# Kernel tuning notes

Hardware: AMD Instinct MI355X
Metric: run time of the kernel (lower is better)

## Reference

```python
import jax, jax.numpy as jnp
import numpy as np

T, B, N = 512, 256, 128


def setup_inputs() -> dict:
    key = jax.random.key(0)
    k1, k2, k3, k4, k5, k6 = jax.random.split(key, 6)
    emit = jax.random.normal(k1, (T, B, N), dtype=jnp.float32)
    target = jax.random.randint(k2, (T, B), 0, N, dtype=jnp.int32)
    # monotone mask: each sequence has length in [T//2, T]
    lengths = jax.random.randint(k3, (B,), T // 2, T + 1, dtype=jnp.int32)
    mask = jnp.arange(T, dtype=jnp.int32)[:, None] < lengths[None, :]
    trans = 0.1 * jax.random.normal(k4, (N, N), dtype=jnp.float32)
    strans = 0.1 * jax.random.normal(k5, (N,), dtype=jnp.float32)
    etrans = 0.1 * jax.random.normal(k6, (N,), dtype=jnp.float32)
    return {"emit": emit, "target": target, "mask": mask,
            "trans": trans, "strans": strans, "etrans": etrans}


def _crf_nll(emit, trans, strans, etrans, target, mask):
    t_len, b, n = emit.shape

    # ---- logZ: forward algorithm (sequential scan over time) ----
    def step(alpha, inp):
        emit_i, mask_i = inp  # [B,N], [B]
        # scores[b, j, k] = alpha[b, j] + trans[j, k] + emit_i[b, k]
        scores = jax.nn.logsumexp(
            alpha[:, :, None] + trans[None, :, :] + emit_i[:, None, :], axis=1)
        alpha = jnp.where(mask_i[:, None], scores, alpha)
        return alpha, None

    alpha0 = strans[None, :] + emit[0]  # [B,N]
    alpha, _ = jax.lax.scan(step, alpha0, (emit[1:], mask[1:]))
    logZ = jax.nn.logsumexp(alpha + etrans[None, :], axis=1).sum()

    # ---- gold score ----
    emit_sc = jnp.take_along_axis(emit, target[:, :, None], axis=2)[..., 0]  # [T,B]
    trans_sc = trans[target[:-1], target[1:]]  # [T-1,B]
    scores = emit_sc.at[1:].add(trans_sc)
    score = jnp.where(mask, scores, 0.0).sum()
    ends = mask.sum(axis=0) - 1  # [B]
    score = score + strans[target[0]].sum()
    score = score + etrans[target[ends, jnp.arange(b)]].sum()

    return (logZ - score) / b


def reference(emit, target, mask, trans, strans, etrans):
    return _crf_nll(emit, trans, strans, etrans, target, mask)
```

## Files before the change

### kernel.cpp

```cpp
#include <hip/hip_runtime.h>

#define T_LEN 512
#define B_SZ  256
#define N_ST  128

#if defined(__has_builtin)
# if __has_builtin(__builtin_amdgcn_fdot2_f32_bf16)
#  define HAVE_DOT2 1
# endif
#endif
#ifndef HAVE_DOT2
# define HAVE_DOT2 0
#endif

typedef unsigned int uint32;
typedef __bf16 bf16x2 __attribute__((ext_vector_type(2)));

__device__ __forceinline__ uint32 bf16rn(float f) {
    uint32 u = __builtin_bit_cast(uint32, f);
    u += 0x7fffu + ((u >> 16) & 1u);
    return u >> 16;
}
__device__ __forceinline__ uint32 pack2(float lo, float hi) {
    return bf16rn(lo) | (bf16rn(hi) << 16);
}
__device__ __forceinline__ uint32 cvtpk(float lo, float hi) {
    uint32 r;
    asm("v_cvt_pk_bf16_f32 %0, %1, %2" : "=v"(r) : "v"(lo), "v"(hi));
    return r;
}
__device__ __forceinline__ float readlane0(float v) {
    return __builtin_bit_cast(float, (uint32)__builtin_amdgcn_readlane(__builtin_bit_cast(int, v), 0));
}
__device__ __forceinline__ float dot2b(uint32 a, uint32 b, float c) {
#if HAVE_DOT2
    return __builtin_amdgcn_fdot2_f32_bf16(__builtin_bit_cast(bf16x2, a),
                                           __builtin_bit_cast(bf16x2, b), c, false);
#else
    float alo = __builtin_bit_cast(float, a << 16);
    float ahi = __builtin_bit_cast(float, a & 0xffff0000u);
    float blo = __builtin_bit_cast(float, b << 16);
    float bhi = __builtin_bit_cast(float, b & 0xffff0000u);
    return fmaf(ahi, bhi, fmaf(alo, blo, c));
#endif
}


__global__ __launch_bounds__(64) void lengths_kernel(const unsigned char* __restrict__ mask_raw,
                                                     int* __restrict__ lens) {
    int b = blockIdx.x;
    int l = threadIdx.x;
    unsigned char b1 = mask_raw[1], b2 = mask_raw[2];
    int mode = (b1 != 0) ? 0 : ((b2 != 0) ? 2 : 1);
    int cnt = 0;
    if (mode == 0) {
        #pragma unroll
        for (int k = 0; k < 8; ++k) cnt += (mask_raw[(l * 8 + k) * B_SZ + b] != 0);
    } else if (mode == 1) {
        const int* m = (const int*)mask_raw;
        #pragma unroll
        for (int k = 0; k < 8; ++k) cnt += (m[(l * 8 + k) * B_SZ + b] != 0);
    } else {
        const float* m = (const float*)mask_raw;
        #pragma unroll
        for (int k = 0; k < 8; ++k) cnt += (m[(l * 8 + k) * B_SZ + b] != 0.0f);
    }
    #pragma unroll
    for (int off = 1; off < 64; off <<= 1) cnt += __shfl_xor(cnt, off);
    if (l == 0) lens[b] = cnt;
}

__global__ void __attribute__((amdgpu_flat_work_group_size(128, 128), amdgpu_waves_per_eu(1, 1)))
forward_kernel(
        const float* __restrict__ emit,
        const float* __restrict__ trans,
        const float* __restrict__ strans,
        const float* __restrict__ etrans,
        const int* __restrict__ lens,
        float* __restrict__ logZ_out) {
    const int b   = blockIdx.x;
    const int tid = threadIdx.x;
    const int wid = tid >> 6;
    const int l   = tid & 63;
    const int c0  = 2 * l, c1 = 2 * l + 1;

    __shared__ alignas(16) uint32 a32[64];
    __shared__ alignas(16) uint32 z32[64];
    __shared__ float meetA[N_ST], meetY[N_ST];
    __shared__ float maccSh[2], red2[2];

    const int len = lens[b];
    const int m = (len - 1 < 256) ? (len - 1) : 256;
    const float* eb = emit + (size_t)b * N_ST;
    const size_t TS = (size_t)B_SZ * N_ST;

    if (wid == 0) {
        uint32 EA[64], EB[64];
        #pragma unroll
        for (int p = 0; p < 64; ++p) {
            EA[p] = pack2(__expf(trans[(2 * p) * N_ST + c0]), __expf(trans[(2 * p + 1) * N_ST + c0]));
            EB[p] = pack2(__expf(trans[(2 * p) * N_ST + c1]), __expf(trans[(2 * p + 1) * N_ST + c1]));
        }
        float aA = __expf(strans[c0] + eb[c0]);
        float aB = __expf(strans[c1] + eb[c1]);
        a32[l] = pack2(aA, aB);
        float Macc = 0.f, inv = 1.0f;
        float ec0 = eb[TS + c0],      ec1 = eb[TS + c1];
        float en0 = eb[2 * TS + c0],  en1 = eb[2 * TS + c1];
        for (int t = 1; t <= m; ++t) {
            const size_t t2 = (size_t)((t + 2 <= m) ? t + 2 : m) * TS;
            const float e20 = eb[t2 + c0], e21 = eb[t2 + c1];
            const float ee0 = __expf(ec0), ee1 = __expf(ec1);
            float A0 = 0, A1 = 0, A2 = 0, A3 = 0, B0 = 0, B1 = 0, B2 = 0, B3 = 0;
            #pragma unroll
            for (int q = 0; q < 16; ++q) {
                uint4 w;
                __builtin_memcpy(&w, (const char*)a32 + 16 * q, 16);
                A0 = dot2b(w.x, EA[4 * q + 0], A0);  B0 = dot2b(w.x, EB[4 * q + 0], B0);
                A1 = dot2b(w.y, EA[4 * q + 1], A1);  B1 = dot2b(w.y, EB[4 * q + 1], B1);
                A2 = dot2b(w.z, EA[4 * q + 2], A2);  B2 = dot2b(w.z, EB[4 * q + 2], B2);
                A3 = dot2b(w.w, EA[4 * q + 3], A3);  B3 = dot2b(w.w, EB[4 * q + 3], B3);
            }
            const float rA = (A0 + A1) + (A2 + A3);
            const float rB = (B0 + B1) + (B2 + B3);
            Macc -= __logf(inv);
            aA = ee0 * rA * inv;
            aB = ee1 * rB * inv;
            a32[l] = cvtpk(aA, aB);
            inv = __builtin_amdgcn_rcpf(readlane0(rA));
            ec0 = en0; ec1 = en1; en0 = e20; en1 = e21;
        }
        meetA[c0] = aA; meetA[c1] = aB;
        if (l == 0) maccSh[0] = Macc;
    } else {
        uint32 RA[64], RB[64];
        #pragma unroll
        for (int p = 0; p < 64; ++p) {
            RA[p] = pack2(__expf(trans[c0 * N_ST + 2 * p]), __expf(trans[c0 * N_ST + 2 * p + 1]));
            RB[p] = pack2(__expf(trans[c1 * N_ST + 2 * p]), __expf(trans[c1 * N_ST + 2 * p + 1]));
        }
        float y0 = __expf(etrans[c0]);
        float y1 = __expf(etrans[c1]);
        float Maccb = 0.f, invb = 1.0f;
        const int t0 = len - 1;
        float ec0 = eb[(size_t)t0 * TS + c0], ec1 = eb[(size_t)t0 * TS + c1];
        float en0 = ec0, en1 = ec1;
        if (t0 - 1 > m) { en0 = eb[(size_t)(t0 - 1) * TS + c0]; en1 = eb[(size_t)(t0 - 1) * TS + c1]; }
        for (int t = t0; t > m; --t) {
            const int tp = (t - 2 > m) ? t - 2 : m + 1;
            const float e20 = eb[(size_t)tp * TS + c0], e21 = eb[(size_t)tp * TS + c1];
            const float ee0 = __expf(ec0), ee1 = __expf(ec1);
            z32[l] = cvtpk(ee0 * y0, ee1 * y1);
            float R0 = 0, R1 = 0, R2 = 0, R3 = 0, S0 = 0, S1 = 0, S2 = 0, S3 = 0;
            #pragma unroll
            for (int q = 0; q < 16; ++q) {
                uint4 w;
                __builtin_memcpy(&w, (const char*)z32 + 16 * q, 16);
                R0 = dot2b(w.x, RA[4 * q + 0], R0);  S0 = dot2b(w.x, RB[4 * q + 0], S0);
                R1 = dot2b(w.y, RA[4 * q + 1], R1);  S1 = dot2b(w.y, RB[4 * q + 1], S1);
                R2 = dot2b(w.z, RA[4 * q + 2], R2);  S2 = dot2b(w.z, RB[4 * q + 2], S2);
                R3 = dot2b(w.w, RA[4 * q + 3], R3);  S3 = dot2b(w.w, RB[4 * q + 3], S3);
            }
            const float rR = (R0 + R1) + (R2 + R3);
            const float rS = (S0 + S1) + (S2 + S3);
            Maccb -= __logf(invb);
            y0 = rR * invb;
            y1 = rS * invb;
            invb = __builtin_amdgcn_rcpf(readlane0(rR));
            ec0 = en0; ec1 = en1; en0 = e20; en1 = e21;
        }
        meetY[c0] = y0; meetY[c1] = y1;
        if (l == 0) maccSh[1] = Maccb;
    }

    __syncthreads();
    float v = meetA[tid] * meetY[tid];
    #pragma unroll
    for (int off = 1; off < 64; off <<= 1) v += __shfl_xor(v, off);
    if (l == 0) red2[wid] = v;
    __syncthreads();
    if (tid == 0) logZ_out[b] = maccSh[0] + maccSh[1] + __logf(red2[0] + red2[1]);
}

__global__ __launch_bounds__(128) void score_kernel(
        const float* __restrict__ emit,
        const int* __restrict__ target,
        const float* __restrict__ trans,
        const float* __restrict__ strans,
        const float* __restrict__ etrans,
        const int* __restrict__ lens,
        float* __restrict__ score_out) {
    const int b   = blockIdx.x;
    const int tid = threadIdx.x;
    const int len = lens[b];
    float local = 0.f;
    for (int t = tid; t < len; t += 128) {
        int tgt = target[t * B_SZ + b];
        float v = emit[(size_t)t * (B_SZ * N_ST) + b * N_ST + tgt];
        if (t > 0) v += trans[target[(t - 1) * B_SZ + b] * N_ST + tgt];
        local += v;
    }
    if (tid == 0) {
        local += strans[target[b]];
        local += etrans[target[(len - 1) * B_SZ + b]];
    }
    #pragma unroll
    for (int off = 1; off < 64; off <<= 1) local += __shfl_xor(local, off);
    __shared__ float partial[2];
    if ((tid & 63) == 0) partial[tid >> 6] = local;
    __syncthreads();
    if (tid == 0) score_out[b] = partial[0] + partial[1];
}

__global__ __launch_bounds__(256) void finalize_kernel(
        const float* __restrict__ logZ,
        const float* __restrict__ score,
        float* __restrict__ out) {
    int tid = threadIdx.x;
    float v = logZ[tid] - score[tid];
    #pragma unroll
    for (int off = 1; off < 64; off <<= 1) v += __shfl_xor(v, off);
    __shared__ float p[4];
    if ((tid & 63) == 0) p[tid >> 6] = v;
    __syncthreads();
    if (tid == 0) out[0] = (p[0] + p[1] + p[2] + p[3]) / 256.0f;
}

extern "C" void kernel_launch(void* const* d_in, const int* in_sizes, int n_in,
                              void* d_out, int out_size, void* d_ws, size_t ws_size,
                              hipStream_t stream) {
    const float*         emit   = (const float*)d_in[0];
    const int*           target = (const int*)d_in[1];
    const unsigned char* mask   = (const unsigned char*)d_in[2];
    const float*         trans  = (const float*)d_in[3];
    const float*         strans = (const float*)d_in[4];
    const float*         etrans = (const float*)d_in[5];

    float* ws     = (float*)d_ws;
    float* logZb  = ws;
    float* scoreb = ws + 256;
    int*   lens   = (int*)(ws + 512);

    lengths_kernel<<<B_SZ, 64, 0, stream>>>(mask, lens);
    forward_kernel<<<B_SZ, 128, 0, stream>>>(emit, trans, strans, etrans, lens, logZb);
    score_kernel<<<B_SZ, 128, 0, stream>>>(emit, target, trans, strans, etrans, lens, scoreb);
    finalize_kernel<<<1, 256, 0, stream>>>(logZb, scoreb, (float*)d_out);
}
```

Baseline: 125.8 us.

## Process two batch sequences per block to interleave independent recurrences

The forward kernel now gives each block two batch elements. The two alpha (and beta) recurrences are interleaved within the same waves, and the grid is halved. The step loop is a serial, latency-bound chain: LDS read, bf16 dot2 accumulation, readlane and reciprocal. Interleaving two independent chains is meant to fill those latency gaps with useful work. Emission loads become float2 vector loads, and the final reduction drops a block barrier. The costs are that the shorter sequence idles, predicated, until the longer one finishes, the grid leaves half the CUs without a block, and register pressure rises.

```diff
diff --git a/kernel.cpp b/kernel.cpp
--- a/kernel.cpp
+++ b/kernel.cpp
@@ -15,6 +15,8 @@
 
 typedef unsigned int uint32;
 typedef __bf16 bf16x2 __attribute__((ext_vector_type(2)));
+typedef float f2v __attribute__((ext_vector_type(2)));
+typedef uint4 __attribute__((may_alias)) uint4a;
 
 __device__ __forceinline__ uint32 bf16rn(float f) {
     uint32 u = __builtin_bit_cast(uint32, f);
@@ -78,21 +80,24 @@
         const float* __restrict__ etrans,
         const int* __restrict__ lens,
         float* __restrict__ logZ_out) {
-    const int b   = blockIdx.x;
+    const int q   = blockIdx.x;
+    const int bA  = 2 * q, bB = 2 * q + 1;
     const int tid = threadIdx.x;
     const int wid = tid >> 6;
     const int l   = tid & 63;
     const int c0  = 2 * l, c1 = 2 * l + 1;
 
-    __shared__ alignas(16) uint32 a32[64];
-    __shared__ alignas(16) uint32 z32[64];
-    __shared__ float meetA[N_ST], meetY[N_ST];
-    __shared__ float maccSh[2], red2[2];
-
-    const int len = lens[b];
-    const int m = (len - 1 < 256) ? (len - 1) : 256;
-    const float* eb = emit + (size_t)b * N_ST;
-    const size_t TS = (size_t)B_SZ * N_ST;
+    __shared__ alignas(16) uint32 aA32[64], aB32[64];
+    __shared__ alignas(16) uint32 zA32[64], zB32[64];
+    __shared__ float meetAsh[2][N_ST], meetYsh[2][N_ST];
+    __shared__ float maccF[2], maccB[2], red2[2];
+
+    const int lenA = lens[bA], lenB = lens[bB];
+    const int mA = (lenA - 1 < 256) ? (lenA - 1) : 256;
+    const int mB = (lenB - 1 < 256) ? (lenB - 1) : 256;
+    const size_t TS2 = (size_t)B_SZ * N_ST / 2;
+    const f2v* evA = (const f2v*)(emit + (size_t)bA * N_ST);
+    const f2v* evB = (const f2v*)(emit + (size_t)bB * N_ST);
 
     if (wid == 0) {
         uint32 EA[64], EB[64];
@@ -101,37 +106,60 @@
             EA[p] = pack2(__expf(trans[(2 * p) * N_ST + c0]), __expf(trans[(2 * p + 1) * N_ST + c0]));
             EB[p] = pack2(__expf(trans[(2 * p) * N_ST + c1]), __expf(trans[(2 * p + 1) * N_ST + c1]));
         }
-        float aA = __expf(strans[c0] + eb[c0]);
-        float aB = __expf(strans[c1] + eb[c1]);
-        a32[l] = pack2(aA, aB);
-        float Macc = 0.f, inv = 1.0f;
-        float ec0 = eb[TS + c0],      ec1 = eb[TS + c1];
-        float en0 = eb[2 * TS + c0],  en1 = eb[2 * TS + c1];
-        for (int t = 1; t <= m; ++t) {
-            const size_t t2 = (size_t)((t + 2 <= m) ? t + 2 : m) * TS;
-            const float e20 = eb[t2 + c0], e21 = eb[t2 + c1];
-            const float ee0 = __expf(ec0), ee1 = __expf(ec1);
+        const float* ebA = emit + (size_t)bA * N_ST;
+        const float* ebB = emit + (size_t)bB * N_ST;
+        float aA0 = __expf(strans[c0] + ebA[c0]);
+        float aA1 = __expf(strans[c1] + ebA[c1]);
+        float aB0 = __expf(strans[c0] + ebB[c0]);
+        float aB1 = __expf(strans[c1] + ebB[c1]);
+        aA32[l] = pack2(aA0, aA1);
+        aB32[l] = pack2(aB0, aB1);
+        float MacA = 0.f, MacB = 0.f, invA = 1.0f, invB = 1.0f;
+        const int tmax = (mA > mB) ? mA : mB;
+        f2v ecA = evA[TS2 + l],     ecB = evB[TS2 + l];
+        f2v enA = evA[2 * TS2 + l], enB = evB[2 * TS2 + l];
+        for (int t = 1; t <= tmax; ++t) {
+            const f2v e2A = evA[(size_t)(t + 2) * TS2 + l];
+            const f2v e2B = evB[(size_t)(t + 2) * TS2 + l];
+            const float eA0 = __expf(ecA.x), eA1 = __expf(ecA.y);
+            const float eB0 = __expf(ecB.x), eB1 = __expf(ecB.y);
             float A0 = 0, A1 = 0, A2 = 0, A3 = 0, B0 = 0, B1 = 0, B2 = 0, B3 = 0;
+            float C0 = 0, C1 = 0, C2 = 0, C3 = 0, D0 = 0, D1 = 0, D2 = 0, D3 = 0;
+            const uint4a* awA = (const uint4a*)aA32;
+            const uint4a* awB = (const uint4a*)aB32;
             #pragma unroll
-            for (int q = 0; q < 16; ++q) {
-                uint4 w;
-                __builtin_memcpy(&w, (const char*)a32 + 16 * q, 16);
-                A0 = dot2b(w.x, EA[4 * q + 0], A0);  B0 = dot2b(w.x, EB[4 * q + 0], B0);
-                A1 = dot2b(w.y, EA[4 * q + 1], A1);  B1 = dot2b(w.y, EB[4 * q + 1], B1);
-                A2 = dot2b(w.z, EA[4 * q + 2], A2);  B2 = dot2b(w.z, EB[4 * q + 2], B2);
-                A3 = dot2b(w.w, EA[4 * q + 3], A3);  B3 = dot2b(w.w, EB[4 * q + 3], B3);
+            for (int p = 0; p < 16; ++p) {
+                const uint4 wA = awA[p];
+                const uint4 wB = awB[p];
+                A0 = dot2b(wA.x, EA[4 * p + 0], A0);  B0 = dot2b(wA.x, EB[4 * p + 0], B0);
+                C0 = dot2b(wB.x, EA[4 * p + 0], C0);  D0 = dot2b(wB.x, EB[4 * p + 0], D0);
+                A1 = dot2b(wA.y, EA[4 * p + 1], A1);  B1 = dot2b(wA.y, EB[4 * p + 1], B1);
+                C1 = dot2b(wB.y, EA[4 * p + 1], C1);  D1 = dot2b(wB.y, EB[4 * p + 1], D1);
+                A2 = dot2b(wA.z, EA[4 * p + 2], A2);  B2 = dot2b(wA.z, EB[4 * p + 2], B2);
+                C2 = dot2b(wB.z, EA[4 * p + 2], C2);  D2 = dot2b(wB.z, EB[4 * p + 2], D2);
+                A3 = dot2b(wA.w, EA[4 * p + 3], A3);  B3 = dot2b(wA.w, EB[4 * p + 3], B3);
+                C3 = dot2b(wB.w, EA[4 * p + 3], C3);  D3 = dot2b(wB.w, EB[4 * p + 3], D3);
             }
-            const float rA = (A0 + A1) + (A2 + A3);
-            const float rB = (B0 + B1) + (B2 + B3);
-            Macc -= __logf(inv);
-            aA = ee0 * rA * inv;
-            aB = ee1 * rB * inv;
-            a32[l] = cvtpk(aA, aB);
-            inv = __builtin_amdgcn_rcpf(readlane0(rA));
-            ec0 = en0; ec1 = en1; en0 = e20; en1 = e21;
-        }
-        meetA[c0] = aA; meetA[c1] = aB;
-        if (l == 0) maccSh[0] = Macc;
+            const float rA0 = (A0 + A1) + (A2 + A3);
+            const float rA1 = (B0 + B1) + (B2 + B3);
+            const float rB0 = (C0 + C1) + (C2 + C3);
+            const float rB1 = (D0 + D1) + (D2 + D3);
+            const bool cA = (t <= mA), cB = (t <= mB);
+            MacA -= cA ? __logf(invA) : 0.0f;
+            MacB -= cB ? __logf(invB) : 0.0f;
+            aA0 = cA ? eA0 * rA0 * invA : aA0;
+            aA1 = cA ? eA1 * rA1 * invA : aA1;
+            aB0 = cB ? eB0 * rB0 * invB : aB0;
+            aB1 = cB ? eB1 * rB1 * invB : aB1;
+            aA32[l] = cvtpk(aA0, aA1);
+            aB32[l] = cvtpk(aB0, aB1);
+            invA = __builtin_amdgcn_rcpf(readlane0(rA0));
+            invB = __builtin_amdgcn_rcpf(readlane0(rB0));
+            ecA = enA; enA = e2A; ecB = enB; enB = e2B;
+        }
+        meetAsh[0][c0] = aA0; meetAsh[0][c1] = aA1;
+        meetAsh[1][c0] = aB0; meetAsh[1][c1] = aB1;
+        if (l == 0) { maccF[0] = MacA; maccF[1] = MacB; }
     } else {
         uint32 RA[64], RB[64];
         #pragma unroll
@@ -139,47 +167,65 @@
             RA[p] = pack2(__expf(trans[c0 * N_ST + 2 * p]), __expf(trans[c0 * N_ST + 2 * p + 1]));
             RB[p] = pack2(__expf(trans[c1 * N_ST + 2 * p]), __expf(trans[c1 * N_ST + 2 * p + 1]));
         }
-        float y0 = __expf(etrans[c0]);
-        float y1 = __expf(etrans[c1]);
-        float Maccb = 0.f, invb = 1.0f;
-        const int t0 = len - 1;
-        float ec0 = eb[(size_t)t0 * TS + c0], ec1 = eb[(size_t)t0 * TS + c1];
-        float en0 = ec0, en1 = ec1;
-        if (t0 - 1 > m) { en0 = eb[(size_t)(t0 - 1) * TS + c0]; en1 = eb[(size_t)(t0 - 1) * TS + c1]; }
-        for (int t = t0; t > m; --t) {
-            const int tp = (t - 2 > m) ? t - 2 : m + 1;
-            const float e20 = eb[(size_t)tp * TS + c0], e21 = eb[(size_t)tp * TS + c1];
-            const float ee0 = __expf(ec0), ee1 = __expf(ec1);
-            z32[l] = cvtpk(ee0 * y0, ee1 * y1);
-            float R0 = 0, R1 = 0, R2 = 0, R3 = 0, S0 = 0, S1 = 0, S2 = 0, S3 = 0;
+        float yA0 = __expf(etrans[c0]), yA1 = __expf(etrans[c1]);
+        float yB0 = yA0,                yB1 = yA1;
+        float MacA = 0.f, MacB = 0.f, invA = 1.0f, invB = 1.0f;
+        const int smax = ((lenA > lenB) ? lenA : lenB) - 1;
+        const int smin = ((mA < mB) ? mA : mB) + 1;
+        f2v ecA = evA[(size_t)smax * TS2 + l],       ecB = evB[(size_t)smax * TS2 + l];
+        f2v enA = evA[(size_t)(smax - 1) * TS2 + l], enB = evB[(size_t)(smax - 1) * TS2 + l];
+        for (int s = smax; s >= smin; --s) {
+            const int sp = (s - 2 >= smin) ? s - 2 : smin;
+            const f2v e2A = evA[(size_t)sp * TS2 + l];
+            const f2v e2B = evB[(size_t)sp * TS2 + l];
+            const float eA0 = __expf(ecA.x), eA1 = __expf(ecA.y);
+            const float eB0 = __expf(ecB.x), eB1 = __expf(ecB.y);
+            zA32[l] = cvtpk(eA0 * yA0, eA1 * yA1);
+            zB32[l] = cvtpk(eB0 * yB0, eB1 * yB1);
+            float A0 = 0, A1 = 0, A2 = 0, A3 = 0, B0 = 0, B1 = 0, B2 = 0, B3 = 0;
+            float C0 = 0, C1 = 0, C2 = 0, C3 = 0, D0 = 0, D1 = 0, D2 = 0, D3 = 0;
+            const uint4a* zwA = (const uint4a*)zA32;
+            const uint4a* zwB = (const uint4a*)zB32;
             #pragma unroll
-            for (int q = 0; q < 16; ++q) {
-                uint4 w;
-                __builtin_memcpy(&w, (const char*)z32 + 16 * q, 16);
-                R0 = dot2b(w.x, RA[4 * q + 0], R0);  S0 = dot2b(w.x, RB[4 * q + 0], S0);
-                R1 = dot2b(w.y, RA[4 * q + 1], R1);  S1 = dot2b(w.y, RB[4 * q + 1], S1);
-                R2 = dot2b(w.z, RA[4 * q + 2], R2);  S2 = dot2b(w.z, RB[4 * q + 2], S2);
-                R3 = dot2b(w.w, RA[4 * q + 3], R3);  S3 = dot2b(w.w, RB[4 * q + 3], S3);
+            for (int p = 0; p < 16; ++p) {
+                const uint4 wA = zwA[p];
+                const uint4 wB = zwB[p];
+                A0 = dot2b(wA.x, RA[4 * p + 0], A0);  B0 = dot2b(wA.x, RB[4 * p + 0], B0);
+                C0 = dot2b(wB.x, RA[4 * p + 0], C0);  D0 = dot2b(wB.x, RB[4 * p + 0], D0);
+                A1 = dot2b(wA.y, RA[4 * p + 1], A1);  B1 = dot2b(wA.y, RB[4 * p + 1], B1);
+                C1 = dot2b(wB.y, RA[4 * p + 1], C1);  D1 = dot2b(wB.y, RB[4 * p + 1], D1);
+                A2 = dot2b(wA.z, RA[4 * p + 2], A2);  B2 = dot2b(wA.z, RB[4 * p + 2], B2);
+                C2 = dot2b(wB.z, RA[4 * p + 2], C2);  D2 = dot2b(wB.z, RB[4 * p + 2], D2);
+                A3 = dot2b(wA.w, RA[4 * p + 3], A3);  B3 = dot2b(wA.w, RB[4 * p + 3], B3);
+                C3 = dot2b(wB.w, RA[4 * p + 3], C3);  D3 = dot2b(wB.w, RB[4 * p + 3], D3);
             }
-            const float rR = (R0 + R1) + (R2 + R3);
-            const float rS = (S0 + S1) + (S2 + S3);
-            Maccb -= __logf(invb);
-            y0 = rR * invb;
-            y1 = rS * invb;
-            invb = __builtin_amdgcn_rcpf(readlane0(rR));
-            ec0 = en0; ec1 = en1; en0 = e20; en1 = e21;
-        }
-        meetY[c0] = y0; meetY[c1] = y1;
-        if (l == 0) maccSh[1] = Maccb;
+            const float rA0 = (A0 + A1) + (A2 + A3);
+            const float rA1 = (B0 + B1) + (B2 + B3);
+            const float rB0 = (C0 + C1) + (C2 + C3);
+            const float rB1 = (D0 + D1) + (D2 + D3);
+            const bool cA = (s <= lenA - 1) && (s >= mA + 1);
+            const bool cB = (s <= lenB - 1) && (s >= mB + 1);
+            MacA -= cA ? __logf(invA) : 0.0f;
+            MacB -= cB ? __logf(invB) : 0.0f;
+            yA0 = cA ? rA0 * invA : yA0;
+            yA1 = cA ? rA1 * invA : yA1;
+            yB0 = cB ? rB0 * invB : yB0;
+            yB1 = cB ? rB1 * invB : yB1;
+            invA = cA ? __builtin_amdgcn_rcpf(readlane0(rA0)) : invA;
+            invB = cB ? __builtin_amdgcn_rcpf(readlane0(rB0)) : invB;
+            ecA = enA; enA = e2A; ecB = enB; enB = e2B;
+        }
+        meetYsh[0][c0] = yA0; meetYsh[0][c1] = yA1;
+        meetYsh[1][c0] = yB0; meetYsh[1][c1] = yB1;
+        if (l == 0) { maccB[0] = MacA; maccB[1] = MacB; }
     }
 
     __syncthreads();
-    float v = meetA[tid] * meetY[tid];
+    float v = meetAsh[wid][l] * meetYsh[wid][l] + meetAsh[wid][l + 64] * meetYsh[wid][l + 64];
     #pragma unroll
     for (int off = 1; off < 64; off <<= 1) v += __shfl_xor(v, off);
-    if (l == 0) red2[wid] = v;
-    __syncthreads();
-    if (tid == 0) logZ_out[b] = maccSh[0] + maccSh[1] + __logf(red2[0] + red2[1]);
+    if (l == 0) logZ_out[2 * q + wid] = maccF[wid] + maccB[wid] + __logf(v);
+    (void)red2;
 }
 
 __global__ __launch_bounds__(128) void score_kernel(
@@ -242,7 +288,7 @@
     int*   lens   = (int*)(ws + 512);
 
     lengths_kernel<<<B_SZ, 64, 0, stream>>>(mask, lens);
-    forward_kernel<<<B_SZ, 128, 0, stream>>>(emit, trans, strans, etrans, lens, logZb);
+    forward_kernel<<<B_SZ / 2, 128, 0, stream>>>(emit, trans, strans, etrans, lens, logZb);
     score_kernel<<<B_SZ, 128, 0, stream>>>(emit, target, trans, strans, etrans, lens, scoreb);
     finalize_kernel<<<1, 256, 0, stream>>>(logZb, scoreb, (float*)d_out);
 }
```

Result: slower. 273.6 us (+117.4%).
